# Kernel optimization log

Measured on AMD Instinct MI355X. Metric: run time of the kernel, lower is better.

## Reference

```python
import jax, jax.numpy as jnp
import numpy as np

FORGET_BIAS = 1.0

def _lstm_scan(x_seq, W, b, c0, h0):
    """x_seq: [T, B, D]; W: [D+H, 4H] (gate order i,j,f,o as in BasicLSTMCell)."""
    def step(carry, x_t):
        c, h = carry
        gates = jnp.dot(jnp.concatenate([x_t, h], axis=-1), W) + b  # [B, 4H]
        i, j, f, o = jnp.split(gates, 4, axis=-1)
        c_new = c * jax.nn.sigmoid(f + FORGET_BIAS) + jax.nn.sigmoid(i) * jnp.tanh(j)
        h_new = jnp.tanh(c_new) * jax.nn.sigmoid(o)
        return (c_new, h_new), h_new
    (c_T, h_T), hs = jax.lax.scan(step, (c0, h0), x_seq)
    return hs, (c_T, h_T)


def setup_inputs() -> dict:
    key = jax.random.key(0)
    ks = jax.random.split(key, 10)
    B, T_enc, D_in = 128, 64, 2048
    T_dec, D_w, H, V = 32, 300, 512, 32000
    s = lambda fan_in: 1.0 / np.sqrt(fan_in)
    return {
        "frames": jax.random.normal(ks[0], (B, T_enc, D_in), dtype=jnp.float32),
        "caption_ids": jax.random.randint(ks[1], (B, T_dec), 0, V, dtype=jnp.int32),
        "emb_table": jax.random.normal(ks[2], (V, D_w), dtype=jnp.float32) * 0.1,
        "W_enc": jax.random.normal(ks[3], (D_in + H, 4 * H), dtype=jnp.float32) * s(D_in + H),
        "b_enc": jnp.zeros((4 * H,), dtype=jnp.float32),
        "W_dec": jax.random.normal(ks[4], (D_w + H, 4 * H), dtype=jnp.float32) * s(D_w + H),
        "b_dec": jnp.zeros((4 * H,), dtype=jnp.float32),
        "W_out": jax.random.normal(ks[5], (H, D_w), dtype=jnp.float32) * s(H),
        "b_out": jnp.zeros((D_w,), dtype=jnp.float32),
    }


def reference(frames, caption_ids, emb_table, W_enc, b_enc, W_dec, b_dec, W_out, b_out):
    B, _, _ = frames.shape
    H = W_out.shape[0]
    c0 = jnp.zeros((B, H), dtype=frames.dtype)
    h0 = jnp.zeros((B, H), dtype=frames.dtype)

    # Encoder: dynamic_rnn over frames (dropout keep_prob=1 -> identity)
    _, enc_state = _lstm_scan(jnp.swapaxes(frames, 0, 1), W_enc, b_enc, c0, h0)

    # Decoder: teacher-forced over caption embeddings, starting from encoder state
    cap_emb = emb_table[caption_ids]                       # [B, T_dec, D_w]
    dec_hs, _ = _lstm_scan(jnp.swapaxes(cap_emb, 0, 1), W_dec, b_dec, *enc_state)  # [T_dec, B, H]

    # hidden_to_word dense per timestep
    word_vecs = jnp.einsum('tbh,hw->tbw', dec_hs, W_out) + b_out  # [T_dec, B, D_w]
    return jnp.swapaxes(word_vecs, 0, 1)                   # [B, T_dec, D_w]
```

## Files before the change

kernel.cpp:

```cpp
#include <hip/hip_runtime.h>
#include <stdint.h>

typedef unsigned short u16;
typedef __attribute__((ext_vector_type(4))) float f32x4;
typedef __attribute__((ext_vector_type(8))) short short8;
typedef __attribute__((ext_vector_type(4))) unsigned short u16x4;
typedef __attribute__((ext_vector_type(4))) int int4v;
typedef __attribute__((ext_vector_type(2))) int int2v;

__device__ __forceinline__ u16 f2b(float f) {
  uint32_t u = __float_as_uint(f);
  uint32_t r = (u + 0x7fffu + ((u >> 16) & 1u)) >> 16;
  return (u16)r;
}
__device__ __forceinline__ float b2f(u16 b) {
  return __uint_as_float(((uint32_t)b) << 16);
}
__device__ __forceinline__ float sigm(float x) { return 1.f / (1.f + __expf(-x)); }
__device__ __forceinline__ float tanh_fast(float x) {
  float e = __expf(2.f * x);
  return 1.f - 2.f / (e + 1.f);
}
__device__ __forceinline__ void gl2lds16(const void* g, void* l) {
  __builtin_amdgcn_global_load_lds((const __attribute__((address_space(1))) void*)g,
                                   (__attribute__((address_space(3))) void*)l, 16, 0, 0);
}

__global__ __launch_bounds__(256)
void prep_kernel(const float* __restrict__ frames, u16* __restrict__ A_enc,
                 const float* __restrict__ W_enc, u16* __restrict__ WencT,
                 const float* __restrict__ W_dec, u16* __restrict__ WdecT,
                 const float* __restrict__ W_out, u16* __restrict__ WoutT,
                 const int* __restrict__ ids, const float* __restrict__ emb,
                 u16* __restrict__ Adec) {
  __shared__ float tile[64][65];
  const int bid = blockIdx.x;
  const int tid = threadIdx.x;

  if (bid < 16384) {
    int i = bid * 256 + tid;
    float4 v = ((const float4*)frames)[i];
    int e = i * 4;
    int b = e >> 17;
    int t = (e >> 11) & 63;
    int d = e & 2047;
    size_t row = (size_t)t * 128 + b;
    u16x4 o = { f2b(v.x), f2b(v.y), f2b(v.z), f2b(v.w) };
    *(u16x4*)(A_enc + row * 2048 + d) = o;
    return;
  }

  const float* W; u16* WT; int ldin, ldout, xreal, xpad, bx, by;
  if (bid < 18080) {
    if (bid < 17664) {
      int idx = bid - 16384;
      W = W_enc; WT = WencT; ldin = 2048; ldout = 2560; xreal = 2048; xpad = 2048;
      bx = idx % 40; by = idx / 40;
    } else {
      int idx = bid - 17664;
      W = W_dec; WT = WdecT; ldin = 2048; ldout = 832; xreal = 300; xpad = 320;
      bx = idx % 13; by = idx / 13;
    }
    const int kb = bx * 64;
    const int pb = by * 64;
    const int pc = tid & 63;
    const int kr4 = tid >> 6;
#pragma unroll
    for (int it = 0; it < 16; ++it) {
      int kl = kr4 + it * 4;
      int kc = kb + kl;
      int ko = kc < xpad ? kc : kc - (xpad - xreal);
      bool valid = (kc < xreal) || (kc >= xpad);
      tile[kl][pc] = valid ? W[(size_t)ko * ldin + pb + pc] : 0.f;
    }
    __syncthreads();
    const int pl = tid >> 2;
    const int kq = tid & 3;
#pragma unroll
    for (int half = 0; half < 2; ++half) {
      union { short8 v; u16 a[8]; } pk;
#pragma unroll
      for (int i = 0; i < 8; ++i) pk.a[i] = f2b(tile[kq * 16 + half * 8 + i][pl]);
      *(short8*)&WT[(size_t)(pb + pl) * ldout + kb + kq * 16 + half * 8] = pk.v;
    }
    return;
  }

  if (bid < 18848) {
    int idx = (bid - 18080) * 256 + tid;
    int n = idx >> 9, k = idx & 511;
    float v = (n < 300) ? W_out[(size_t)k * 300 + n] : 0.f;
    WoutT[idx] = f2b(v);
    return;
  }

  int r = (bid - 18848) * 4 + (tid >> 6);
  int t = r >> 7, b = r & 127;
  int id = ids[b * 32 + t];
  const float* src = emb + (size_t)id * 300;
  u16* dst = Adec + (size_t)r * 320;
  for (int d = tid & 63; d < 320; d += 64)
    dst[d] = f2b(d < 300 ? src[d] : 0.f);
}

struct SmemLstm { u16 wlds[128][520]; u16 stage[2][16][32]; };
struct SmemGemm { u16 at[4][128 * 32]; u16 bt[4][128 * 32]; };
union SmemU { SmemLstm l; SmemGemm g; };

__global__ __launch_bounds__(256)
void mega_kernel(const u16* __restrict__ A_enc, const u16* __restrict__ WencT,
                 u16* __restrict__ pre_enc, const float* __restrict__ b_enc,
                 const u16* __restrict__ A_dec, const u16* __restrict__ WdecT,
                 u16* __restrict__ pre_dec, const float* __restrict__ b_dec,
                 const u16* __restrict__ WoutT, const float* __restrict__ b_out,
                 float* __restrict__ outp,
                 int* __restrict__ hbuf, u16* __restrict__ dec_hs,
                 int* __restrict__ flags, int* __restrict__ pf_enc,
                 int* __restrict__ pf_dec, int* __restrict__ dflags) {
  __shared__ SmemU sm;
  const int bid = blockIdx.x;
  const int tid = threadIdx.x;
  const int lane = tid & 63;

  if (bid < 128) {
    const int hb = tid >> 6;
    const int bg = bid & 7;
    const int hg = bid >> 3;
    const int colq = lane & 15;
    const int rquad = lane >> 4;

    for (int i = tid; i < 128 * 64; i += 256) {
      int lr = i >> 6, cc = i & 63;
      const u16* src = WencT + (size_t)((lr >> 5) * 512 + hg * 32 + (lr & 31)) * 2560 + 2048;
      *(short8*)&sm.l.wlds[lr][cc * 8] = *(const short8*)(src + cc * 8);
    }
    __syncthreads();

    float cst[4] = {0.f, 0.f, 0.f, 0.f};
    const int brow = bg * 16 + rquad * 4;
    const size_t pchunk = ((((size_t)(bg * 16 + hg) * 2 + (hb & 1)) * 4 + rquad) * 16 + colq) * 16;
    union HV { int4v i; short8 s; };
    union PR { int4v i; u16 a[8]; };
    int pf_next = 0;

    for (int s = 0; s < 96; ++s) {
      const bool dec = (s >= 64);
      const int sb = s & 1;
      if (hb < 2) {
        const u16* pre_t = dec ? (pre_dec + (size_t)(s - 64) * 262144)
                               : (pre_enc + (size_t)s * 262144);
        if (pf_next != 16) {
          int* pf = dec ? (pf_dec + (s - 64)) : (pf_enc + s);
          while (__hip_atomic_load(pf, __ATOMIC_RELAXED, __HIP_MEMORY_SCOPE_AGENT) != 16)
            __builtin_amdgcn_s_sleep(1);
        }
        asm volatile("" ::: "memory");
        PR praw[2];
        const u16* p0 = pre_t + pchunk;
        asm volatile("global_load_dwordx4 %0, %1, off sc0 sc1"
                     : "=v"(praw[0].i) : "v"(p0) : "memory");
        asm volatile("global_load_dwordx4 %0, %1, off offset:16 sc0 sc1"
                     : "=v"(praw[1].i) : "v"(p0) : "memory");
        if (s > 0) {
          const int* fp = flags + ((size_t)s * 8 + bg) * 16 + (lane & 15);
          while (__hip_atomic_load(fp, __ATOMIC_RELAXED, __HIP_MEMORY_SCOPE_AGENT) == 0) {}
          asm volatile("" ::: "memory");
        }
        HV hv[16];
        const int* hread = hbuf + (size_t)s * 32768 + bg * 4096 + colq * 16 + rquad * 4;
#pragma unroll
        for (int g = 0; g < 4; ++g) {
          const int* hp = hread + g * 1024;
#pragma unroll
          for (int q = 0; q < 4; ++q)
            asm volatile("global_load_dwordx4 %0, %1, off offset:%2 sc0 sc1"
                         : "=v"(hv[g * 4 + q].i) : "v"(hp), "i"(q * 1024) : "memory");
        }
        if (s + 1 < 96) {
          const int* pfn = (s + 1 >= 64) ? (pf_dec + (s + 1 - 64)) : (pf_enc + (s + 1));
          pf_next = __hip_atomic_load(pfn, __ATOMIC_RELAXED, __HIP_MEMORY_SCOPE_AGENT);
        }
        asm volatile("s_waitcnt vmcnt(0)" ::: "memory");
        __builtin_amdgcn_sched_barrier(0);
#pragma unroll
        for (int kt = 0; kt < 16; ++kt) asm volatile("" : "+v"(hv[kt].i));
        asm volatile("" : "+v"(praw[0].i), "+v"(praw[1].i));
        f32x4 acc[4];
#pragma unroll
        for (int l = 0; l < 4; ++l)
#pragma unroll
          for (int r = 0; r < 4; ++r) {
            int e = l * 4 + r;
            acc[l][r] = b2f(praw[e >> 3].a[e & 7]);
          }
#pragma unroll
        for (int kt = 0; kt < 16; ++kt) {
#pragma unroll
          for (int l = 0; l < 4; ++l) {
            short8 bf = *(const short8*)&sm.l.wlds[l * 32 + hb * 16 + colq][kt * 32 + rquad * 8];
            acc[l] = __builtin_amdgcn_mfma_f32_16x16x32_bf16(hv[kt].s, bf, acc[l], 0, 0, 0);
          }
        }
#pragma unroll
        for (int r = 0; r < 4; ++r) {
          float iv = acc[0][r], jv = acc[1][r], fv = acc[2][r], ov = acc[3][r];
          float cn = cst[r] * sigm(fv + 1.f) + sigm(iv) * tanh_fast(jv);
          cst[r] = cn;
          float hvv = tanh_fast(cn) * sigm(ov);
          sm.l.stage[sb][rquad * 4 + r][hb * 16 + colq] = f2b(hvv);
        }
      }
      __syncthreads();
      if (hb == 2) {
        const int t2 = tid - 128;
        const int row = t2 >> 2, q = t2 & 3;
        union { short8 v; int4v i; } vv;
        vv.v = *(const short8*)&sm.l.stage[sb][row][q * 8];
        int* dst = hbuf + (size_t)(s + 1) * 32768 + bg * 4096 + hg * 256 + row * 16 + q * 4;
        asm volatile("global_store_dwordx4 %0, %1, off sc0 sc1"
                     :: "v"(dst), "v"(vv.i) : "memory");
        if (dec) {
          const u16* da = dec_hs + (size_t)(s - 64) * 65536 +
                          (size_t)(bg * 16 + row) * 512 + hg * 32 + q * 8;
          asm volatile("global_store_dwordx4 %0, %1, off sc0 sc1"
                       :: "v"(da), "v"(vv.i) : "memory");
        }
        asm volatile("s_waitcnt vmcnt(0)" ::: "memory");
        if (t2 == 0) {
          int* fp = flags + ((size_t)(s + 1) * 8 + bg) * 16 + hg;
          int one = 1;
          asm volatile("global_store_dword %0, %1, off sc0 sc1"
                       :: "v"(fp), "v"(one) : "memory");
        }
        if (dec && t2 == 1) {
          int* dfp = dflags + (size_t)(s - 64) * 128 + bid;
          int one = 1;
          asm volatile("global_store_dword %0, %1, off sc0 sc1"
                       :: "v"(dfp), "v"(one) : "memory");
        }
      }
      if (s == 63) {
        for (int i = tid; i < 128 * 64; i += 256) {
          int lr = i >> 6, cc = i & 63;
          const u16* src = WdecT + (size_t)((lr >> 5) * 512 + hg * 32 + (lr & 31)) * 832 + 320;
          *(short8*)&sm.l.wlds[lr][cc * 8] = *(const short8*)(src + cc * 8);
        }
        __syncthreads();
      }
    }
    asm volatile("s_waitcnt vmcnt(0)" ::: "memory");
    return;
  }

  int idx = bid - 128;
  const u16* A; const u16* BT; u16* Cb = nullptr; const float* bias; int* flag = nullptr;
  int lda, ldb, K, m0, n0, mode;
  if (idx < 1024) {
    int t = idx >> 4, nt = idx & 15;
    A = A_enc; lda = 2048; BT = WencT; ldb = 2560; K = 2048;
    Cb = pre_enc + (size_t)t * 262144; bias = b_enc; flag = pf_enc + t;
    m0 = t * 128; n0 = nt * 128; mode = 0;
  } else if (idx < 1536) {
    idx -= 1024;
    int t = idx >> 4, nt = idx & 15;
    A = A_dec; lda = 320; BT = WdecT; ldb = 832; K = 320;
    Cb = pre_dec + (size_t)t * 262144; bias = b_dec; flag = pf_dec + t;
    m0 = t * 128; n0 = nt * 128; mode = 0;
  } else {
    idx -= 1536;
    int t = idx / 3, nt = idx % 3;
    A = dec_hs; lda = 512; BT = WoutT; ldb = 512; K = 512;
    bias = b_out; m0 = t * 128; n0 = nt * 128; mode = 1;
    if (tid < 128) {
      const int* wf = dflags + (size_t)t * 128 + tid;
      while (__hip_atomic_load(wf, __ATOMIC_RELAXED, __HIP_MEMORY_SCOPE_AGENT) == 0)
        __builtin_amdgcn_s_sleep(8);
    }
    asm volatile("" ::: "memory");
    __syncthreads();
  }
  const int wave = tid >> 6;
  const int wm = wave & 1, wn = wave >> 1;
  const int colq = lane & 15, rquad = lane >> 4;

  f32x4 acc[4][4];
#pragma unroll
  for (int i = 0; i < 4; ++i)
#pragma unroll
    for (int j = 0; j < 4; ++j) { f32x4 z = {0.f, 0.f, 0.f, 0.f}; acc[i][j] = z; }

  auto stage_tile = [&](int buf, int k0) {
#pragma unroll
    for (int c = 0; c < 2; ++c) {
      const int ch = wave + c * 4;
      const int slot = ch * 64 + lane;
      const int m = slot >> 2;
      const int koff = (slot & 3) * 8;
      gl2lds16(A + (size_t)(m0 + m) * lda + k0 + koff, sm.g.at[buf] + ch * 512);
      gl2lds16(BT + (size_t)(n0 + m) * ldb + k0 + koff, sm.g.bt[buf] + ch * 512);
    }
  };

  const int niter = K >> 5;
  stage_tile(0, 0);
  stage_tile(1, 32);
  stage_tile(2, 64);
  for (int it = 0; it < niter; ++it) {
    if (it + 3 < niter) stage_tile((it + 3) & 3, (it + 3) << 5);
    const int excess = (niter - 1 - it) < 3 ? (niter - 1 - it) : 3;
    if (excess == 3)      asm volatile("s_waitcnt vmcnt(12)" ::: "memory");
    else if (excess == 2) asm volatile("s_waitcnt vmcnt(8)" ::: "memory");
    else if (excess == 1) asm volatile("s_waitcnt vmcnt(4)" ::: "memory");
    else                  asm volatile("s_waitcnt vmcnt(0)" ::: "memory");
    __builtin_amdgcn_s_barrier();
    __builtin_amdgcn_sched_barrier(0);
    const int cur = it & 3;
    short8 af[4], bf[4];
#pragma unroll
    for (int i = 0; i < 4; ++i)
      af[i] = *(const short8*)(sm.g.at[cur] + (wm * 64 + i * 16 + colq) * 32 + rquad * 8);
#pragma unroll
    for (int j = 0; j < 4; ++j)
      bf[j] = *(const short8*)(sm.g.bt[cur] + (wn * 64 + j * 16 + colq) * 32 + rquad * 8);
#pragma unroll
    for (int i = 0; i < 4; ++i)
#pragma unroll
      for (int j = 0; j < 4; ++j)
        acc[i][j] = __builtin_amdgcn_mfma_f32_16x16x32_bf16(af[i], bf[j], acc[i][j], 0, 0, 0);
    __builtin_amdgcn_sched_barrier(0);
    asm volatile("s_waitcnt lgkmcnt(0)" ::: "memory");
    __builtin_amdgcn_s_barrier();
  }

  const int gm_base = m0 + wm * 64;
  const int gn_base = n0 + wn * 64;
  if (mode == 0) {
#pragma unroll
    for (int i = 0; i < 4; ++i) {
      const int bgp = wm * 4 + i;
#pragma unroll
      for (int j = 0; j < 4; ++j) {
        const int gnb = gn_base + j * 16;
        const int gn = gnb + colq;
        const float bv = bias[gn];
        const int l = gnb >> 9;
        const int hcolb = gnb & 511;
        const int hg_ = hcolb >> 5;
        const int hb_ = (hcolb >> 4) & 1;
        u16* cp = Cb + ((((size_t)(bgp * 16 + hg_) * 2 + hb_) * 4 + rquad) * 16 + colq) * 16
                     + l * 4;
        union { u16x4 h; int2v d; } pk;
#pragma unroll
        for (int r = 0; r < 4; ++r) pk.h[r] = f2b(acc[i][j][r] + bv);
        asm volatile("global_store_dwordx2 %0, %1, off sc0 sc1"
                     :: "v"(cp), "v"(pk.d) : "memory");
      }
    }
    asm volatile("s_waitcnt vmcnt(0)" ::: "memory");
    __syncthreads();
    if (tid == 0)
      __hip_atomic_fetch_add(flag, 1, __ATOMIC_RELAXED, __HIP_MEMORY_SCOPE_AGENT);
  } else {
#pragma unroll
    for (int i = 0; i < 4; ++i) {
#pragma unroll
      for (int j = 0; j < 4; ++j) {
        const int gn = gn_base + j * 16 + colq;
        const float bv = (gn < 300) ? bias[gn] : 0.f;
        const int rbase = gm_base + i * 16 + rquad * 4;
#pragma unroll
        for (int r = 0; r < 4; ++r) {
          const float v = acc[i][j][r] + bv;
          const int row = rbase + r;
          if (gn < 300)
            outp[(size_t)((row & 127) * 32 + (row >> 7)) * 300 + gn] = v;
        }
      }
    }
  }
}

extern "C" void kernel_launch(void* const* d_in, const int* in_sizes, int n_in,
                              void* d_out, int out_size, void* d_ws, size_t ws_size,
                              hipStream_t stream) {
  const float* frames = (const float*)d_in[0];
  const int* cap_ids  = (const int*)d_in[1];
  const float* emb    = (const float*)d_in[2];
  const float* W_enc  = (const float*)d_in[3];
  const float* b_enc  = (const float*)d_in[4];
  const float* W_dec  = (const float*)d_in[5];
  const float* b_dec  = (const float*)d_in[6];
  const float* W_out  = (const float*)d_in[7];
  const float* b_out  = (const float*)d_in[8];
  float* out = (float*)d_out;

  char* ws = (char*)d_ws;
  size_t off = 0;
  auto alloc = [&](size_t bytes) {
    void* p = ws + off;
    off += (bytes + 255) & ~(size_t)255;
    return p;
  };
  u16* A_enc   = (u16*)alloc(8192ull * 2048 * 2);
  u16* WencT   = (u16*)alloc(2048ull * 2560 * 2);
  u16* pre_enc = (u16*)alloc(64ull * 128 * 2048 * 2);
  u16* A_dec   = (u16*)alloc(4096ull * 320 * 2);
  u16* WdecT   = (u16*)alloc(2048ull * 832 * 2);
  u16* pre_dec = (u16*)alloc(32ull * 128 * 2048 * 2);
  u16* WoutT   = (u16*)alloc(384ull * 512 * 2);
  u16* dec_hs  = (u16*)alloc(32ull * 128 * 512 * 2);
  int* hbuf    = (int*)alloc(97ull * 32768 * 4);
  int* flags   = (int*)alloc(97ull * 8 * 16 * 4);
  int* pf      = (int*)alloc(96ull * 4);
  int* dflags  = (int*)alloc(32ull * 128 * 4);
  int* pf_enc  = pf;
  int* pf_dec  = pf + 64;

  hipMemsetAsync(hbuf, 0, 32768ull * 4, stream);
  hipMemsetAsync(flags, 0, 97ull * 8 * 16 * 4, stream);
  hipMemsetAsync(pf, 0, 96ull * 4, stream);
  hipMemsetAsync(dflags, 0, 32ull * 128 * 4, stream);

  prep_kernel<<<19872, 256, 0, stream>>>(frames, A_enc, W_enc, WencT, W_dec, WdecT,
                                         W_out, WoutT, cap_ids, emb, A_dec);

  mega_kernel<<<1760, 256, 0, stream>>>(A_enc, WencT, pre_enc, b_enc,
                                        A_dec, WdecT, pre_dec, b_dec,
                                        WoutT, b_out, out,
                                        hbuf, dec_hs, flags, pf_enc, pf_dec, dflags);
}
```

Baseline: 664.9 us.

## Probe L2 sharing among recurrent blocks and use sc0-only coherence when safe

At the start of the recurrent phase the 128 LSTM blocks run a runtime probe, using a global barrier and magic-value stores, to check whether each batch-group's 16 peer blocks can see each other's writes through non-system-scope (sc0-only) memory ops. When every peer passes, the per-step hidden-state exchange and flag spinning use sc0 loads and stores instead of sc0 sc1. This is meant to cut latency on the serial 96-step critical path. A periodic fallback poll of a separate system-scope flag array covers the sc0 path, and flag arrays are padded to 64 ints per group to spread them out. The cost is extra startup barriers and the risk of stale reads if the probe's conclusion does not hold.

```diff
diff --git a/kernel.cpp b/kernel.cpp
--- a/kernel.cpp
+++ b/kernel.cpp
@@ -115,9 +115,13 @@
                  const u16* __restrict__ WoutT, const float* __restrict__ b_out,
                  float* __restrict__ outp,
                  int* __restrict__ hbuf, u16* __restrict__ dec_hs,
-                 int* __restrict__ flags, int* __restrict__ pf_enc,
-                 int* __restrict__ pf_dec, int* __restrict__ dflags) {
+                 int* __restrict__ flags, int* __restrict__ mflags,
+                 int* __restrict__ pf_enc, int* __restrict__ pf_dec,
+                 int* __restrict__ dflags, int* __restrict__ probe1,
+                 int* __restrict__ probe2, int* __restrict__ verd,
+                 int* __restrict__ xcnt) {
   __shared__ SmemU sm;
+  __shared__ int hs_fast;
   const int bid = blockIdx.x;
   const int tid = threadIdx.x;
   const int lane = tid & 63;
@@ -134,10 +138,83 @@
       const u16* src = WencT + (size_t)((lr >> 5) * 512 + hg * 32 + (lr & 31)) * 2560 + 2048;
       *(short8*)&sm.l.wlds[lr][cc * 8] = *(const short8*)(src + cc * 8);
     }
-    __syncthreads();
+
+    {
+      int* scr = (int*)&sm.l.stage[0][0][0];
+      auto bar128 = [&](int k) {
+        __hip_atomic_fetch_add(xcnt + k, 1, __ATOMIC_RELAXED, __HIP_MEMORY_SCOPE_AGENT);
+        while (__hip_atomic_load(xcnt + k, __ATOMIC_RELAXED, __HIP_MEMORY_SCOPE_AGENT) != 128)
+          __builtin_amdgcn_s_sleep(2);
+      };
+      if (tid == 0) {
+        int* pp = probe1 + bid * 64;
+        int magic = 0x5EED0001;
+        asm volatile("global_store_dword %0, %1, off sc0" :: "v"(pp), "v"(magic) : "memory");
+        asm volatile("s_waitcnt vmcnt(0)" ::: "memory");
+        bar128(0);
+      }
+      __syncthreads();
+      if (tid < 16) {
+        const int* pp = probe1 + (tid * 8 + bg) * 64;
+        int seen = 0;
+        for (int itp = 0; itp < 64 && !seen; ++itp) {
+          int v;
+          asm volatile("global_load_dword %0, %1, off sc0\n\ts_waitcnt vmcnt(0)"
+                       : "=v"(v) : "v"(pp) : "memory");
+          seen = (v == 0x5EED0001);
+        }
+        scr[tid] = seen;
+      }
+      __syncthreads();
+      if (tid < 16) {
+        const int* pp = probe2 + (tid * 8 + bg) * 64;
+        int v;
+        asm volatile("global_load_dword %0, %1, off sc0\n\ts_waitcnt vmcnt(0)"
+                     : "=v"(v) : "v"(pp) : "memory");
+        scr[64] = (scr[64] & 0) | v;
+      }
+      __syncthreads();
+      if (tid == 0) {
+        bar128(1);
+        int* pp = probe2 + bid * 64;
+        int magic = 0x5EED0002;
+        asm volatile("global_store_dword %0, %1, off sc0" :: "v"(pp), "v"(magic) : "memory");
+        asm volatile("s_waitcnt vmcnt(0)" ::: "memory");
+        bar128(2);
+      }
+      __syncthreads();
+      if (tid < 16) {
+        const int* pp = probe2 + (tid * 8 + bg) * 64;
+        int seen = 0;
+        for (int itp = 0; itp < 64 && !seen; ++itp) {
+          int v;
+          asm volatile("global_load_dword %0, %1, off sc0\n\ts_waitcnt vmcnt(0)"
+                       : "=v"(v) : "v"(pp) : "memory");
+          seen = (v == 0x5EED0002);
+        }
+        scr[16 + tid] = seen;
+      }
+      __syncthreads();
+      if (tid == 0) {
+        int ok = 1;
+        for (int j = 0; j < 16; ++j) if (!scr[j] || !scr[16 + j]) ok = 0;
+        int myok = ok ? 2 : 1;
+        int* vp = verd + bid;
+        asm volatile("global_store_dword %0, %1, off sc0 sc1"
+                     :: "v"(vp), "v"(myok) : "memory");
+        asm volatile("s_waitcnt vmcnt(0)" ::: "memory");
+        bar128(3);
+        int f = 1;
+        for (int j = 0; j < 16; ++j)
+          if (__hip_atomic_load(verd + (j * 8 + bg), __ATOMIC_RELAXED,
+                                __HIP_MEMORY_SCOPE_AGENT) != 2) f = 0;
+        hs_fast = f;
+      }
+      __syncthreads();
+    }
+    const int fast = hs_fast;
 
     float cst[4] = {0.f, 0.f, 0.f, 0.f};
-    const int brow = bg * 16 + rquad * 4;
     const size_t pchunk = ((((size_t)(bg * 16 + hg) * 2 + (hb & 1)) * 4 + rquad) * 16 + colq) * 16;
     union HV { int4v i; short8 s; };
     union PR { int4v i; u16 a[8]; };
@@ -162,19 +239,46 @@
         asm volatile("global_load_dwordx4 %0, %1, off offset:16 sc0 sc1"
                      : "=v"(praw[1].i) : "v"(p0) : "memory");
         if (s > 0) {
-          const int* fp = flags + ((size_t)s * 8 + bg) * 16 + (lane & 15);
-          while (__hip_atomic_load(fp, __ATOMIC_RELAXED, __HIP_MEMORY_SCOPE_AGENT) == 0) {}
+          const size_t freg = ((size_t)s * 8 + bg) * 64 + (lane & 15);
+          const int* fp = flags + freg;
+          if (fast) {
+            const int* mfp = mflags + freg;
+            int fv = 0, tries = 0;
+            do {
+              if ((tries & 63) == 63) {
+                asm volatile("global_load_dword %0, %1, off sc0 sc1\n\ts_waitcnt vmcnt(0)"
+                             : "=v"(fv) : "v"(mfp) : "memory");
+              } else {
+                asm volatile("global_load_dword %0, %1, off sc0\n\ts_waitcnt vmcnt(0)"
+                             : "=v"(fv) : "v"(fp) : "memory");
+              }
+              ++tries;
+            } while (fv == 0);
+          } else {
+            while (__hip_atomic_load(fp, __ATOMIC_RELAXED, __HIP_MEMORY_SCOPE_AGENT) == 0) {}
+          }
           asm volatile("" ::: "memory");
         }
         HV hv[16];
         const int* hread = hbuf + (size_t)s * 32768 + bg * 4096 + colq * 16 + rquad * 4;
-#pragma unroll
-        for (int g = 0; g < 4; ++g) {
-          const int* hp = hread + g * 1024;
-#pragma unroll
-          for (int q = 0; q < 4; ++q)
-            asm volatile("global_load_dwordx4 %0, %1, off offset:%2 sc0 sc1"
-                         : "=v"(hv[g * 4 + q].i) : "v"(hp), "i"(q * 1024) : "memory");
+        if (fast) {
+#pragma unroll
+          for (int g = 0; g < 4; ++g) {
+            const int* hp = hread + g * 1024;
+#pragma unroll
+            for (int q = 0; q < 4; ++q)
+              asm volatile("global_load_dwordx4 %0, %1, off offset:%2 sc0"
+                           : "=v"(hv[g * 4 + q].i) : "v"(hp), "i"(q * 1024) : "memory");
+          }
+        } else {
+#pragma unroll
+          for (int g = 0; g < 4; ++g) {
+            const int* hp = hread + g * 1024;
+#pragma unroll
+            for (int q = 0; q < 4; ++q)
+              asm volatile("global_load_dwordx4 %0, %1, off offset:%2 sc0 sc1"
+                           : "=v"(hv[g * 4 + q].i) : "v"(hp), "i"(q * 1024) : "memory");
+          }
         }
         if (s + 1 < 96) {
           const int* pfn = (s + 1 >= 64) ? (pf_dec + (s + 1 - 64)) : (pf_enc + (s + 1));
@@ -217,26 +321,43 @@
         union { short8 v; int4v i; } vv;
         vv.v = *(const short8*)&sm.l.stage[sb][row][q * 8];
         int* dst = hbuf + (size_t)(s + 1) * 32768 + bg * 4096 + hg * 256 + row * 16 + q * 4;
-        asm volatile("global_store_dwordx4 %0, %1, off sc0 sc1"
-                     :: "v"(dst), "v"(vv.i) : "memory");
+        const size_t freg = ((size_t)(s + 1) * 8 + bg) * 64 + hg;
+        if (fast) {
+          asm volatile("global_store_dwordx4 %0, %1, off sc0"
+                       :: "v"(dst), "v"(vv.i) : "memory");
+          asm volatile("s_waitcnt vmcnt(0)" ::: "memory");
+          if (t2 == 0) {
+            int one = 1;
+            int* fp = flags + freg;
+            int* mfp = mflags + freg;
+            asm volatile("global_store_dword %0, %1, off sc0"
+                         :: "v"(fp), "v"(one) : "memory");
+            asm volatile("global_store_dword %0, %1, off sc0 sc1"
+                         :: "v"(mfp), "v"(one) : "memory");
+          }
+        } else {
+          asm volatile("global_store_dwordx4 %0, %1, off sc0 sc1"
+                       :: "v"(dst), "v"(vv.i) : "memory");
+          asm volatile("s_waitcnt vmcnt(0)" ::: "memory");
+          if (t2 == 0) {
+            int one = 1;
+            int* fp = flags + freg;
+            asm volatile("global_store_dword %0, %1, off sc0 sc1"
+                         :: "v"(fp), "v"(one) : "memory");
+          }
+        }
         if (dec) {
           const u16* da = dec_hs + (size_t)(s - 64) * 65536 +
                           (size_t)(bg * 16 + row) * 512 + hg * 32 + q * 8;
           asm volatile("global_store_dwordx4 %0, %1, off sc0 sc1"
                        :: "v"(da), "v"(vv.i) : "memory");
-        }
-        asm volatile("s_waitcnt vmcnt(0)" ::: "memory");
-        if (t2 == 0) {
-          int* fp = flags + ((size_t)(s + 1) * 8 + bg) * 16 + hg;
-          int one = 1;
-          asm volatile("global_store_dword %0, %1, off sc0 sc1"
-                       :: "v"(fp), "v"(one) : "memory");
-        }
-        if (dec && t2 == 1) {
-          int* dfp = dflags + (size_t)(s - 64) * 128 + bid;
-          int one = 1;
-          asm volatile("global_store_dword %0, %1, off sc0 sc1"
-                       :: "v"(dfp), "v"(one) : "memory");
+          asm volatile("s_waitcnt vmcnt(0)" ::: "memory");
+          if (t2 == 1) {
+            int* dfp = dflags + (size_t)(s - 64) * 128 + bid;
+            int one = 1;
+            asm volatile("global_store_dword %0, %1, off sc0 sc1"
+                         :: "v"(dfp), "v"(one) : "memory");
+          }
         }
       }
       if (s == 63) {
@@ -410,16 +531,26 @@
   u16* WoutT   = (u16*)alloc(384ull * 512 * 2);
   u16* dec_hs  = (u16*)alloc(32ull * 128 * 512 * 2);
   int* hbuf    = (int*)alloc(97ull * 32768 * 4);
-  int* flags   = (int*)alloc(97ull * 8 * 16 * 4);
+  int* flags   = (int*)alloc(97ull * 8 * 64 * 4);
+  int* mflags  = (int*)alloc(97ull * 8 * 64 * 4);
   int* pf      = (int*)alloc(96ull * 4);
   int* dflags  = (int*)alloc(32ull * 128 * 4);
+  int* probe1  = (int*)alloc(128ull * 64 * 4);
+  int* probe2  = (int*)alloc(128ull * 64 * 4);
+  int* verd    = (int*)alloc(128ull * 4);
+  int* xcnt    = (int*)alloc(8ull * 4);
   int* pf_enc  = pf;
   int* pf_dec  = pf + 64;
 
   hipMemsetAsync(hbuf, 0, 32768ull * 4, stream);
-  hipMemsetAsync(flags, 0, 97ull * 8 * 16 * 4, stream);
+  hipMemsetAsync(flags, 0, 97ull * 8 * 64 * 4, stream);
+  hipMemsetAsync(mflags, 0, 97ull * 8 * 64 * 4, stream);
   hipMemsetAsync(pf, 0, 96ull * 4, stream);
   hipMemsetAsync(dflags, 0, 32ull * 128 * 4, stream);
+  hipMemsetAsync(probe1, 0, 128ull * 64 * 4, stream);
+  hipMemsetAsync(probe2, 0, 128ull * 64 * 4, stream);
+  hipMemsetAsync(verd, 0, 128ull * 4, stream);
+  hipMemsetAsync(xcnt, 0, 8ull * 4, stream);
 
   prep_kernel<<<19872, 256, 0, stream>>>(frames, A_enc, W_enc, WencT, W_dec, WdecT,
                                          W_out, WoutT, cap_ids, emb, A_dec);
@@ -427,5 +558,7 @@
   mega_kernel<<<1760, 256, 0, stream>>>(A_enc, WencT, pre_enc, b_enc,
                                         A_dec, WdecT, pre_dec, b_dec,
                                         WoutT, b_out, out,
-                                        hbuf, dec_hs, flags, pf_enc, pf_dec, dflags);
-}
+                                        hbuf, dec_hs, flags, mflags,
+                                        pf_enc, pf_dec, dflags,
+                                        probe1, probe2, verd, xcnt);
+}
```

Measured after the change: 773.9 us. 16.4% more time.
